# Kernel tuning notes

Hardware: AMD Instinct MI355X
Metric: run time of the kernel (lower is better)

The kernel has to match this reference:

```python
import jax, jax.numpy as jnp
import numpy as np
import math

B, SEQ, H, HKV, D = 2, 2048, 32, 8, 128
BLOCK, LOCAL_BLOCKS, VERT_STRIDE = 64, 16, 8
NB = SEQ // BLOCK


def _build_layout():
    # local + vertical-strided causal block-sparse layout (homo heads),
    # converted from CSR to a padded [NB, max_nnz] column-index table.
    q_idx = np.arange(NB)[:, None]
    k_idx = np.arange(NB)[None, :]
    dense = (k_idx <= q_idx) & ((q_idx - k_idx < LOCAL_BLOCKS) | ((k_idx + 1) % VERT_STRIDE == 0))
    max_nnz = int(dense.sum(1).max())  # == 18 for NB=32, local=16, stride=8
    cols = np.zeros((NB, max_nnz), np.int32)
    valid = np.zeros((NB, max_nnz), np.bool_)
    for i in range(NB):
        c = np.nonzero(dense[i])[0]
        cols[i, :c.size] = c
        valid[i, :c.size] = True
    return jnp.asarray(cols), jnp.asarray(valid)


def setup_inputs() -> dict:
    key = jax.random.key(0)
    kq, kk, kv = jax.random.split(key, 3)
    q = jax.random.normal(kq, (B, SEQ, H, D), jnp.float32)
    k = jax.random.normal(kk, (B, SEQ, HKV, D), jnp.float32)
    v = jax.random.normal(kv, (B, SEQ, HKV, D), jnp.float32)
    layout_cols, layout_mask = _build_layout()
    return {"q": q, "k": k, "v": v, "layout_cols": layout_cols, "layout_mask": layout_mask}


def _attn(q, k, v, layout_cols, layout_mask):
    Bn, S, Hq, Dh = q.shape
    Hkv = k.shape[2]
    g = Hq // Hkv               # GQA group size (q_k_ratio)
    nb, nnz = layout_cols.shape
    blk = S // nb               # block_size
    sm_scale = 1.0 / math.sqrt(Dh)
    # reshape to blocks; keep KV at Hkv heads (no repeat) and group q heads
    qb = q.reshape(Bn, nb, blk, Hkv, g, Dh).transpose(0, 3, 4, 1, 2, 5)  # [B,Hkv,g,nb,blk,D]
    kb = k.reshape(Bn, nb, blk, Hkv, Dh).transpose(0, 3, 1, 2, 4)        # [B,Hkv,nb,blk,D]
    vb = v.reshape(Bn, nb, blk, Hkv, Dh).transpose(0, 3, 1, 2, 4)
    # gather only the attended K/V blocks per query block (honors block sparsity)
    kg = jnp.take(kb, layout_cols, axis=2)  # [B,Hkv,nb,nnz,blk,D]
    vg = jnp.take(vb, layout_cols, axis=2)
    scores = jnp.einsum('bhgqmd,bhqknd->bhgqmkn', qb, kg) * sm_scale  # [B,Hkv,g,nb,blk,nnz,blk]
    # token-level causal mask + padded-column mask (past_len = 0 for prefill)
    q_tok = jnp.arange(nb)[:, None] * blk + jnp.arange(blk)[None, :]            # [nb,blk]
    k_tok = layout_cols[:, :, None] * blk + jnp.arange(blk)[None, None, :]      # [nb,nnz,blk]
    valid = layout_mask[:, None, :, None] & (k_tok[:, None] <= q_tok[:, :, None, None])  # [nb,blk,nnz,blk]
    scores = jnp.where(valid[None, None, None], scores, -jnp.inf)
    p = jax.nn.softmax(scores.reshape(Bn, Hkv, g, nb, blk, nnz * blk), axis=-1).reshape(scores.shape)
    out = jnp.einsum('bhgqmkn,bhqknd->bhgqmd', p, vg)
    return out.transpose(0, 3, 4, 1, 2, 5).reshape(Bn, S, Hq, Dh)


def reference(q, k, v, layout_cols, layout_mask):
    return _attn(q, k, v, layout_cols, layout_mask)
```

## Files before the change

kernel.cpp:

```cpp
#include <hip/hip_runtime.h>

#define B_    2
#define SEQ_  2048
#define H_    32
#define HKV_  8
#define D_    128
#define BLK_  64
#define NB_   32
#define LOCAL_ 16
#define VERT_  8

#define PSTR 72
#define NTASK 512
#define NBLOCK 256

typedef __attribute__((ext_vector_type(8))) short bf16x8;
typedef __attribute__((ext_vector_type(4))) float f32x4;
typedef __attribute__((ext_vector_type(16))) float f32x16;

__device__ __forceinline__ unsigned short f2bf(float f) {
    union { float f; unsigned u; } x; x.f = f;
    unsigned u = x.u;
    return (unsigned short)((u + 0x7FFFu + ((u >> 16) & 1u)) >> 16);
}

__device__ __forceinline__ unsigned pk2(float a, float b) {
#if defined(__has_builtin) && __has_builtin(__builtin_amdgcn_cvt_pk_bf16_f32)
    typedef __attribute__((ext_vector_type(2))) __bf16 bf2;
    bf2 r = __builtin_amdgcn_cvt_pk_bf16_f32(a, b);
    unsigned u; __builtin_memcpy(&u, &r, 4); return u;
#else
    return (unsigned)f2bf(a) | ((unsigned)f2bf(b) << 16);
#endif
}

__device__ __forceinline__ void pswap(unsigned &a, unsigned &b) {
#if defined(__has_builtin) && __has_builtin(__builtin_amdgcn_permlane32_swap)
    auto r = __builtin_amdgcn_permlane32_swap((int)a, (int)b, false, false);
    a = (unsigned)r[0]; b = (unsigned)r[1];
#else
    asm("v_permlane32_swap_b32 %0, %1" : "+v"(a), "+v"(b));
#endif
}

__device__ __forceinline__ f32x16 zero16() {
    f32x16 z;
#pragma unroll
    for (int i = 0; i < 16; ++i) z[i] = 0.f;
    return z;
}

__device__ __forceinline__ int next_valid(int qb, int j) {
    for (++j; j <= qb; ++j)
        if (((qb - j) < LOCAL_) || (((j + 1) & (VERT_ - 1)) == 0)) return j;
    return qb + 1;
}

__device__ __forceinline__ void dma16(const unsigned short* g, unsigned short* l) {
    __builtin_amdgcn_global_load_lds(
        (const __attribute__((address_space(1))) unsigned int*)g,
        (__attribute__((address_space(3))) unsigned int*)l, 16, 0, 0);
}

__global__ __launch_bounds__(256)
void prepass_kernel(const float* __restrict__ kg, const float* __restrict__ vg,
                    unsigned short* __restrict__ Kws, unsigned short* __restrict__ Vws) {
    __shared__ unsigned short Vt[D_ * 72];
    const int bid = blockIdx.x;
    const int b   = bid >> 8;
    const int hkv = (bid >> 5) & 7;
    const int jb  = bid & 31;
    const int tid = threadIdx.x;
    const int rs  = HKV_ * D_;

    const float* kbase = kg + ((size_t)(b * SEQ_ + jb * BLK_) * HKV_ + hkv) * D_;
    const float* vbase = vg + ((size_t)(b * SEQ_ + jb * BLK_) * HKV_ + hkv) * D_;
    unsigned short* Kdst = Kws + ((size_t)(b * 8 + hkv) * SEQ_ + jb * BLK_) * D_;
    unsigned short* Vdst = Vws + ((size_t)(b * 8 + hkv) * NB_ + jb) * (D_ * BLK_);

#pragma unroll
    for (int t = 0; t < 4; ++t) {
        const int q = t * 256 + tid;
        const int row = q >> 4, c = q & 15;
        const float* p = kbase + (size_t)row * rs + c * 8;
        const float4 a = *(const float4*)p;
        const float4 d4 = *(const float4*)(p + 4);
        uint4 u = { pk2(a.x, a.y), pk2(a.z, a.w), pk2(d4.x, d4.y), pk2(d4.z, d4.w) };
        *(uint4*)&Kdst[row * 128 + ((c ^ (row & 15)) << 3)] = u;
    }
#pragma unroll
    for (int t = 0; t < 8; ++t) {
        const int q = t * 256 + tid;
        const int pos = q >> 5, c4 = q & 31;
        const float4 v4 = *(const float4*)(vbase + (size_t)pos * rs + c4 * 4);
        const unsigned u0 = pk2(v4.x, v4.y), u1 = pk2(v4.z, v4.w);
        Vt[(c4 * 4 + 0) * 72 + pos] = (unsigned short)u0;
        Vt[(c4 * 4 + 1) * 72 + pos] = (unsigned short)(u0 >> 16);
        Vt[(c4 * 4 + 2) * 72 + pos] = (unsigned short)u1;
        Vt[(c4 * 4 + 3) * 72 + pos] = (unsigned short)(u1 >> 16);
    }
    __syncthreads();
#pragma unroll
    for (int t = 0; t < 4; ++t) {
        const int q = t * 256 + tid;
        const int d = q >> 3, c = q & 7;
        const uint2 q0 = *(const uint2*)&Vt[d * 72 + c * 8];
        const uint2 q1 = *(const uint2*)&Vt[d * 72 + c * 8 + 4];
        uint4 u = { q0.x, q0.y, q1.x, q1.y };
        *(uint4*)&Vdst[d * 64 + ((c ^ (d & 7)) << 3)] = u;
    }
}

__global__ __launch_bounds__(512, 2)
void sparse_attn_v3(const float* __restrict__ qg, float* __restrict__ outg,
                    const unsigned short* __restrict__ Kws,
                    const unsigned short* __restrict__ Vws,
                    unsigned* __restrict__ ctr) {
    __shared__ __align__(16) unsigned short Kb[2][BLK_ * D_];
    __shared__ __align__(16) unsigned short Vb[2][D_ * BLK_];
    __shared__ unsigned taskLds;

    const int tid  = threadIdx.x;
    const int wave = tid >> 6;
    const int lane = tid & 63;
    const int q5   = lane & 31;
    const int h    = lane >> 5;
    const int hsub = wave >> 1;
    const int rt2  = wave & 1;

    int cskA[8];
#pragma unroll
    for (int dk = 0; dk < 8; ++dk) cskA[dk] = ((((dk * 2) | h) ^ (lane & 15)) << 3);
    int csvB[4];
#pragma unroll
    for (int kc = 0; kc < 4; ++kc) csvB[kc] = ((((kc * 2) | h) ^ (lane & 7)) << 3);

    const float c2 = 0.12751649736230723f;
    const short oneb = (short)0x3F80;
    const bf16x8 ones = {oneb, oneb, oneb, oneb, oneb, oneb, oneb, oneb};

    for (;;) {
        __syncthreads();
        if (tid == 0) taskLds = atomicAdd(ctr, 1u);
        __syncthreads();
        const unsigned t = taskLds;
        if (t >= NTASK) break;

        const int qb  = 31 - (int)(t >> 4);
        const int bh  = (int)(t & 15);
        const int b   = bh >> 3;
        const int hkv = bh & 7;
        const int head = hkv * 4 + hsub;

        const unsigned short* Kbh = Kws + (size_t)(b * 8 + hkv) * SEQ_ * D_;
        const unsigned short* Vbh = Vws + (size_t)(b * 8 + hkv) * NB_ * (D_ * BLK_);

        int j = next_valid(qb, -1);
        {
            const size_t off = (size_t)j * (BLK_ * D_);
#pragma unroll
            for (int i = 0; i < 2; ++i) {
                dma16(Kbh + off + i * 4096 + tid * 8, &Kb[0][i * 4096 + wave * 512]);
                dma16(Vbh + off + i * 4096 + tid * 8, &Vb[0][i * 4096 + wave * 512]);
            }
        }

        bf16x8 qf[8];
        {
            const int row = qb * BLK_ + rt2 * 32 + q5;
            const float* qp = qg + ((size_t)(b * SEQ_ + row) * H_ + head) * D_ + h * 8;
#pragma unroll
            for (int dk = 0; dk < 8; ++dk) {
                const float4 a = *(const float4*)(qp + dk * 16);
                const float4 c = *(const float4*)(qp + dk * 16 + 4);
                uint4 u = { pk2(a.x, a.y), pk2(a.z, a.w), pk2(c.x, c.y), pk2(c.z, c.w) };
                __builtin_memcpy(&qf[dk], &u, 16);
            }
        }

        f32x16 lacc = zero16();
        f32x16 o_acc[4];
#pragma unroll
        for (int dt = 0; dt < 4; ++dt) o_acc[dt] = zero16();

        __syncthreads();
        int it = 0;
        while (j <= qb) {
            const int jn = next_valid(qb, j);
            const int cur = it & 1;
            if (jn <= qb) {
                const size_t off = (size_t)jn * (BLK_ * D_);
#pragma unroll
                for (int i = 0; i < 2; ++i) {
                    dma16(Kbh + off + i * 4096 + tid * 8, &Kb[cur ^ 1][i * 4096 + wave * 512]);
                    dma16(Vbh + off + i * 4096 + tid * 8, &Vb[cur ^ 1][i * 4096 + wave * 512]);
                }
            }

            const bool diag  = (j == qb);
            const bool diagw = diag && (rt2 == 0);

            const unsigned short* kb = Kb[cur];
            f32x16 s0 = zero16(), s1 = zero16();
            {
                const unsigned short* k0r = kb + q5 * 128;
                const unsigned short* k1r = kb + (32 + q5) * 128;
#pragma unroll
                for (int dk = 0; dk < 8; ++dk) {
                    const bf16x8 kf0 = *(const bf16x8*)(k0r + cskA[dk]);
                    s0 = __builtin_amdgcn_mfma_f32_32x32x16_bf16(kf0, qf[dk], s0, 0, 0, 0);
                }
                if (!diagw) {
#pragma unroll
                    for (int dk = 0; dk < 8; ++dk) {
                        const bf16x8 kf1 = *(const bf16x8*)(k1r + cskA[dk]);
                        s1 = __builtin_amdgcn_mfma_f32_32x32x16_bf16(kf1, qf[dk], s1, 0, 0, 0);
                    }
                }
            }

            if (diag) {
                if (rt2 == 0) {
#pragma unroll
                    for (int r = 0; r < 16; ++r) {
                        const int crow = (r & 3) + 8 * (r >> 2) + 4 * h;
                        if (crow > q5) s0[r] = -INFINITY;
                    }
                } else {
#pragma unroll
                    for (int r = 0; r < 16; ++r) {
                        const int crow = (r & 3) + 8 * (r >> 2) + 4 * h;
                        if (crow > q5) s1[r] = -INFINITY;
                    }
                }
            }

#pragma unroll
            for (int r = 0; r < 16; ++r) s0[r] = exp2f(s0[r] * c2);
            if (!diagw) {
#pragma unroll
                for (int r = 0; r < 16; ++r) s1[r] = exp2f(s1[r] * c2);
            }

            bf16x8 pa[4];
#pragma unroll
            for (int kc = 0; kc < 4; ++kc) {
                if (kc >= 2 && diagw) continue;
                const f32x16 &pp = (kc >= 2) ? s1 : s0;
                const int b0 = (kc & 1) * 8;
                unsigned A0 = pk2(pp[b0 + 0], pp[b0 + 1]);
                unsigned B0 = pk2(pp[b0 + 4], pp[b0 + 5]);
                unsigned A1 = pk2(pp[b0 + 2], pp[b0 + 3]);
                unsigned B1 = pk2(pp[b0 + 6], pp[b0 + 7]);
                pswap(A0, B0);
                pswap(A1, B1);
                uint4 u = { A0, A1, B0, B1 };
                __builtin_memcpy(&pa[kc], &u, 16);
                lacc = __builtin_amdgcn_mfma_f32_32x32x16_bf16(pa[kc], ones, lacc, 0, 0, 0);
            }

            const unsigned short* vb = Vb[cur];
#pragma unroll
            for (int dt = 0; dt < 4; ++dt) {
                const unsigned short* vrow = vb + (dt * 32 + q5) * 64;
#pragma unroll
                for (int kc = 0; kc < 4; ++kc) {
                    if (kc >= 2 && diagw) continue;
                    const bf16x8 vf = *(const bf16x8*)(vrow + csvB[kc]);
                    o_acc[dt] = __builtin_amdgcn_mfma_f32_32x32x16_bf16(pa[kc], vf, o_acc[dt], 0, 0, 0);
                }
            }

            __syncthreads();
            j = jn; ++it;
        }

        const int rowbase = qb * BLK_ + rt2 * 32;
#pragma unroll
        for (int r = 0; r < 16; ++r) {
            const int row = rowbase + (r & 3) + 8 * (r >> 2) + 4 * h;
            const float inv = 1.0f / lacc[r];
            float* op = outg + ((size_t)(b * SEQ_ + row) * H_ + head) * D_ + q5;
            op[0]  = o_acc[0][r] * inv;
            op[32] = o_acc[1][r] * inv;
            op[64] = o_acc[2][r] * inv;
            op[96] = o_acc[3][r] * inv;
        }
    }
}

#define KSTR 136
#define VSTR 72
__global__ __launch_bounds__(1024)
void sparse_attn_v1(const float* __restrict__ qg, const float* __restrict__ kg,
                    const float* __restrict__ vg, float* __restrict__ outg,
                    unsigned* __restrict__ ctr) {
    __shared__ __align__(16) unsigned short Klds[BLK_ * KSTR];
    __shared__ __align__(16) unsigned short Vlds[D_ * VSTR];
    __shared__ __align__(16) unsigned short Plds[16 * 16 * PSTR];
    __shared__ unsigned taskLds;

    const int tid  = threadIdx.x;
    const int wave = tid >> 6;
    const int lane = tid & 63;
    const int l15  = lane & 15;
    const int quad = lane >> 4;
    const int hsub = wave >> 2;
    const int rt   = wave & 3;

    const int srow0 = tid >> 5, srow1 = srow0 + 32;
    const int sc4   = tid & 31;
    const int kld0  = srow0 * KSTR + sc4 * 4, kld1 = srow1 * KSTR + sc4 * 4;
    const int vd    = sc4 * 4;
    const int vskew = (sc4 & 7) << 3;
    const int vp0   = (srow0 + vskew) & 63, vp1 = (srow1 + vskew) & 63;
    const size_t stoff0 = (size_t)srow0 * (HKV_ * D_) + sc4 * 4;
    const size_t stoff1 = (size_t)srow1 * (HKV_ * D_) + sc4 * 4;

    const float c2 = 0.12751649736230723f;
    const short oneb = (short)0x3F80;
    const bf16x8 ones = {oneb, oneb, oneb, oneb, oneb, oneb, oneb, oneb};
    unsigned short* pl = &Plds[wave * 16 * PSTR];

    for (;;) {
        __syncthreads();
        if (tid == 0) taskLds = atomicAdd(ctr, 1u);
        __syncthreads();
        const unsigned t = taskLds;
        if (t >= NTASK) break;
        const int qb  = 31 - (int)(t >> 4);
        const int bh  = (int)(t & 15);
        const int b   = bh >> 3;
        const int hkv = bh & 7;
        const int head = hkv * 4 + hsub;
        const float* kbase = kg + ((size_t)(b * SEQ_) * HKV_ + hkv) * D_;
        const float* vbase = vg + ((size_t)(b * SEQ_) * HKV_ + hkv) * D_;
        bf16x8 qf[4];
        {
            const int row = qb * BLK_ + rt * 16 + l15;
            const float* qp = qg + ((size_t)(b * SEQ_ + row) * H_ + head) * D_;
#pragma unroll
            for (int s = 0; s < 4; ++s) {
                const float4 a = *(const float4*)(qp + s * 32 + quad * 8);
                const float4 c = *(const float4*)(qp + s * 32 + quad * 8 + 4);
                uint4 u = { pk2(a.x, a.y), pk2(a.z, a.w), pk2(c.x, c.y), pk2(c.z, c.w) };
                __builtin_memcpy(&qf[s], &u, 16);
            }
        }
        f32x4 lacc = f32x4{0.f, 0.f, 0.f, 0.f};
        f32x4 o_acc[8];
#pragma unroll
        for (int t8 = 0; t8 < 8; ++t8) o_acc[t8] = f32x4{0.f, 0.f, 0.f, 0.f};
        int j = next_valid(qb, -1);
        float4 kpr0, kpr1, vpr0, vpr1;
        {
            const float* kp = kbase + (size_t)j * BLK_ * HKV_ * D_;
            const float* vp = vbase + (size_t)j * BLK_ * HKV_ * D_;
            kpr0 = *(const float4*)(kp + stoff0); kpr1 = *(const float4*)(kp + stoff1);
            vpr0 = *(const float4*)(vp + stoff0); vpr1 = *(const float4*)(vp + stoff1);
        }
        while (j <= qb) {
            const int jn = next_valid(qb, j);
            __syncthreads();
            {
                uint2 u0 = { pk2(kpr0.x, kpr0.y), pk2(kpr0.z, kpr0.w) };
                uint2 u1 = { pk2(kpr1.x, kpr1.y), pk2(kpr1.z, kpr1.w) };
                *(uint2*)&Klds[kld0] = u0;
                *(uint2*)&Klds[kld1] = u1;
                unsigned a0 = pk2(vpr0.x, vpr0.y), a1 = pk2(vpr0.z, vpr0.w);
                Vlds[(vd + 0) * VSTR + vp0] = (unsigned short)a0;
                Vlds[(vd + 1) * VSTR + vp0] = (unsigned short)(a0 >> 16);
                Vlds[(vd + 2) * VSTR + vp0] = (unsigned short)a1;
                Vlds[(vd + 3) * VSTR + vp0] = (unsigned short)(a1 >> 16);
                unsigned b0 = pk2(vpr1.x, vpr1.y), b1 = pk2(vpr1.z, vpr1.w);
                Vlds[(vd + 0) * VSTR + vp1] = (unsigned short)b0;
                Vlds[(vd + 1) * VSTR + vp1] = (unsigned short)(b0 >> 16);
                Vlds[(vd + 2) * VSTR + vp1] = (unsigned short)b1;
                Vlds[(vd + 3) * VSTR + vp1] = (unsigned short)(b1 >> 16);
            }
            __syncthreads();
            if (jn <= qb) {
                const float* kp = kbase + (size_t)jn * BLK_ * HKV_ * D_;
                const float* vp = vbase + (size_t)jn * BLK_ * HKV_ * D_;
                kpr0 = *(const float4*)(kp + stoff0); kpr1 = *(const float4*)(kp + stoff1);
                vpr0 = *(const float4*)(vp + stoff0); vpr1 = *(const float4*)(vp + stoff1);
            }
            f32x4 sacc[4];
#pragma unroll
            for (int t4 = 0; t4 < 4; ++t4) {
                f32x4 acc = f32x4{0.f, 0.f, 0.f, 0.f};
#pragma unroll
                for (int s = 0; s < 4; ++s) {
                    const bf16x8 kf = *(const bf16x8*)&Klds[(t4 * 16 + l15) * KSTR + s * 32 + quad * 8];
                    acc = __builtin_amdgcn_mfma_f32_16x16x32_bf16(qf[s], kf, acc, 0, 0, 0);
                }
                sacc[t4] = acc;
            }
            if (j == qb) {
                const int rowbase = rt * 16 + quad * 4;
#pragma unroll
                for (int t4 = 0; t4 < 4; ++t4) {
                    const int col = t4 * 16 + l15;
#pragma unroll
                    for (int r = 0; r < 4; ++r)
                        if (col > rowbase + r) sacc[t4][r] = -INFINITY;
                }
            }
#pragma unroll
            for (int t4 = 0; t4 < 4; ++t4) {
                const float p0 = exp2f(sacc[t4][0] * c2);
                const float p1 = exp2f(sacc[t4][1] * c2);
                const float p2 = exp2f(sacc[t4][2] * c2);
                const float p3 = exp2f(sacc[t4][3] * c2);
                const unsigned u01 = pk2(p0, p1), u23 = pk2(p2, p3);
                const int cb = t4 * 16 + l15;
                pl[(quad * 4 + 0) * PSTR + cb] = (unsigned short)u01;
                pl[(quad * 4 + 1) * PSTR + cb] = (unsigned short)(u01 >> 16);
                pl[(quad * 4 + 2) * PSTR + cb] = (unsigned short)u23;
                pl[(quad * 4 + 3) * PSTR + cb] = (unsigned short)(u23 >> 16);
            }
#pragma unroll
            for (int s2 = 0; s2 < 2; ++s2) {
                const bf16x8 pf = *(const bf16x8*)&pl[l15 * PSTR + s2 * 32 + quad * 8];
                lacc = __builtin_amdgcn_mfma_f32_16x16x32_bf16(pf, ones, lacc, 0, 0, 0);
                const int k0 = s2 * 32 + quad * 8;
#pragma unroll
                for (int t8 = 0; t8 < 8; ++t8) {
                    const int n  = t8 * 16 + l15;
                    const int p2 = (k0 + (((n >> 2) & 7) << 3)) & 63;
                    const bf16x8 vf = *(const bf16x8*)&Vlds[n * VSTR + p2];
                    o_acc[t8] = __builtin_amdgcn_mfma_f32_16x16x32_bf16(pf, vf, o_acc[t8], 0, 0, 0);
                }
            }
            j = jn;
        }
        const int orow = qb * BLK_ + rt * 16 + quad * 4;
#pragma unroll
        for (int r = 0; r < 4; ++r) {
            const float inv_l = 1.0f / lacc[r];
            float* op = outg + ((size_t)(b * SEQ_ + orow + r) * H_ + head) * D_;
#pragma unroll
            for (int t8 = 0; t8 < 8; ++t8)
                op[t8 * 16 + l15] = o_acc[t8][r] * inv_l;
        }
    }
}

extern "C" void kernel_launch(void* const* d_in, const int* in_sizes, int n_in,
                              void* d_out, int out_size, void* d_ws, size_t ws_size,
                              hipStream_t stream) {
    const float* q = (const float*)d_in[0];
    const float* k = (const float*)d_in[1];
    const float* v = (const float*)d_in[2];
    float* out = (float*)d_out;

    const size_t kws_elems = (size_t)B_ * HKV_ * SEQ_ * D_;
    const size_t need = 256 + 2 * kws_elems * sizeof(unsigned short);
    if (ws_size >= need) {
        unsigned short* Kws = (unsigned short*)((char*)d_ws + 256);
        unsigned short* Vws = Kws + kws_elems;
        hipMemsetAsync(d_ws, 0, 256, stream);
        prepass_kernel<<<dim3(B_ * HKV_ * NB_), dim3(256), 0, stream>>>(k, v, Kws, Vws);
        sparse_attn_v3<<<dim3(NBLOCK), dim3(512), 0, stream>>>(q, out, Kws, Vws, (unsigned*)d_ws);
    } else {
        hipMemsetAsync(d_ws, 0, sizeof(unsigned), stream);
        sparse_attn_v1<<<dim3(NBLOCK), dim3(1024), 0, stream>>>(q, k, v, out, (unsigned*)d_ws);
    }
}
```

Before: 239.8 us.

## Triple-buffer K/V tiles and overlap next QK with current PV

After: 407.7 us. 1.7x slower.

```diff
diff --git a/kernel.cpp b/kernel.cpp
--- a/kernel.cpp
+++ b/kernel.cpp
@@ -112,12 +112,12 @@
 }
 
 __global__ __launch_bounds__(512, 2)
-void sparse_attn_v3(const float* __restrict__ qg, float* __restrict__ outg,
+void sparse_attn_v4(const float* __restrict__ qg, float* __restrict__ outg,
                     const unsigned short* __restrict__ Kws,
                     const unsigned short* __restrict__ Vws,
                     unsigned* __restrict__ ctr) {
-    __shared__ __align__(16) unsigned short Kb[2][BLK_ * D_];
-    __shared__ __align__(16) unsigned short Vb[2][D_ * BLK_];
+    __shared__ __align__(16) unsigned short Kb[3][BLK_ * D_];
+    __shared__ __align__(16) unsigned short Vb[3][D_ * BLK_];
     __shared__ unsigned taskLds;
 
     const int tid  = threadIdx.x;
@@ -155,15 +155,22 @@
         const unsigned short* Kbh = Kws + (size_t)(b * 8 + hkv) * SEQ_ * D_;
         const unsigned short* Vbh = Vws + (size_t)(b * 8 + hkv) * NB_ * (D_ * BLK_);
 
+        auto STAGE = [&](int tile, int buf) {
+            const size_t off = (size_t)tile * (BLK_ * D_);
+#pragma unroll
+            for (int i = 0; i < 2; ++i) {
+                dma16(Kbh + off + i * 4096 + tid * 8, &Kb[buf][i * 4096 + wave * 512]);
+                dma16(Vbh + off + i * 4096 + tid * 8, &Vb[buf][i * 4096 + wave * 512]);
+            }
+        };
+
+        f32x16 lacc = zero16();
+        f32x16 o_acc[4];
+#pragma unroll
+        for (int dt = 0; dt < 4; ++dt) o_acc[dt] = zero16();
+
         int j = next_valid(qb, -1);
-        {
-            const size_t off = (size_t)j * (BLK_ * D_);
-#pragma unroll
-            for (int i = 0; i < 2; ++i) {
-                dma16(Kbh + off + i * 4096 + tid * 8, &Kb[0][i * 4096 + wave * 512]);
-                dma16(Vbh + off + i * 4096 + tid * 8, &Vb[0][i * 4096 + wave * 512]);
-            }
-        }
+        STAGE(j, 0);
 
         bf16x8 qf[8];
         {
@@ -178,47 +185,31 @@
             }
         }
 
-        f32x16 lacc = zero16();
-        f32x16 o_acc[4];
-#pragma unroll
-        for (int dt = 0; dt < 4; ++dt) o_acc[dt] = zero16();
-
-        __syncthreads();
-        int it = 0;
-        while (j <= qb) {
-            const int jn = next_valid(qb, j);
-            const int cur = it & 1;
-            if (jn <= qb) {
-                const size_t off = (size_t)jn * (BLK_ * D_);
-#pragma unroll
-                for (int i = 0; i < 2; ++i) {
-                    dma16(Kbh + off + i * 4096 + tid * 8, &Kb[cur ^ 1][i * 4096 + wave * 512]);
-                    dma16(Vbh + off + i * 4096 + tid * 8, &Vb[cur ^ 1][i * 4096 + wave * 512]);
-                }
-            }
-
-            const bool diag  = (j == qb);
-            const bool diagw = diag && (rt2 == 0);
-
-            const unsigned short* kb = Kb[cur];
-            f32x16 s0 = zero16(), s1 = zero16();
-            {
-                const unsigned short* k0r = kb + q5 * 128;
-                const unsigned short* k1r = kb + (32 + q5) * 128;
+        f32x16 s0, s1;
+        auto QK = [&](int buf, bool skip_hi) {
+            const unsigned short* kb = Kb[buf];
+            const unsigned short* k0r = kb + q5 * 128;
+            const unsigned short* k1r = kb + (32 + q5) * 128;
+            s0 = zero16();
+#pragma unroll
+            for (int dk = 0; dk < 8; ++dk) {
+                const bf16x8 kf0 = *(const bf16x8*)(k0r + cskA[dk]);
+                s0 = __builtin_amdgcn_mfma_f32_32x32x16_bf16(kf0, qf[dk], s0, 0, 0, 0);
+            }
+            if (!skip_hi) {
+                s1 = zero16();
 #pragma unroll
                 for (int dk = 0; dk < 8; ++dk) {
-                    const bf16x8 kf0 = *(const bf16x8*)(k0r + cskA[dk]);
-                    s0 = __builtin_amdgcn_mfma_f32_32x32x16_bf16(kf0, qf[dk], s0, 0, 0, 0);
-                }
-                if (!diagw) {
-#pragma unroll
-                    for (int dk = 0; dk < 8; ++dk) {
-                        const bf16x8 kf1 = *(const bf16x8*)(k1r + cskA[dk]);
-                        s1 = __builtin_amdgcn_mfma_f32_32x32x16_bf16(kf1, qf[dk], s1, 0, 0, 0);
-                    }
-                }
-            }
-
+                    const bf16x8 kf1 = *(const bf16x8*)(k1r + cskA[dk]);
+                    s1 = __builtin_amdgcn_mfma_f32_32x32x16_bf16(kf1, qf[dk], s1, 0, 0, 0);
+                }
+            }
+        };
+
+        bf16x8 pa[4];
+        auto EXPPACK = [&](int jj) {
+            const bool diag = (jj == qb);
+            const bool dw   = diag && (rt2 == 0);
             if (diag) {
                 if (rt2 == 0) {
 #pragma unroll
@@ -234,18 +225,15 @@
                     }
                 }
             }
-
 #pragma unroll
             for (int r = 0; r < 16; ++r) s0[r] = exp2f(s0[r] * c2);
-            if (!diagw) {
+            if (!dw) {
 #pragma unroll
                 for (int r = 0; r < 16; ++r) s1[r] = exp2f(s1[r] * c2);
             }
-
-            bf16x8 pa[4];
 #pragma unroll
             for (int kc = 0; kc < 4; ++kc) {
-                if (kc >= 2 && diagw) continue;
+                if (kc >= 2 && dw) continue;
                 const f32x16 &pp = (kc >= 2) ? s1 : s0;
                 const int b0 = (kc & 1) * 8;
                 unsigned A0 = pk2(pp[b0 + 0], pp[b0 + 1]);
@@ -258,21 +246,37 @@
                 __builtin_memcpy(&pa[kc], &u, 16);
                 lacc = __builtin_amdgcn_mfma_f32_32x32x16_bf16(pa[kc], ones, lacc, 0, 0, 0);
             }
-
-            const unsigned short* vb = Vb[cur];
+        };
+
+        auto PV = [&](int buf, bool dw) {
+            const unsigned short* vb = Vb[buf];
 #pragma unroll
             for (int dt = 0; dt < 4; ++dt) {
                 const unsigned short* vrow = vb + (dt * 32 + q5) * 64;
 #pragma unroll
                 for (int kc = 0; kc < 4; ++kc) {
-                    if (kc >= 2 && diagw) continue;
+                    if (kc >= 2 && dw) continue;
                     const bf16x8 vf = *(const bf16x8*)(vrow + csvB[kc]);
                     o_acc[dt] = __builtin_amdgcn_mfma_f32_32x32x16_bf16(pa[kc], vf, o_acc[dt], 0, 0, 0);
                 }
             }
-
+        };
+
+        int jn = next_valid(qb, j);
+        __syncthreads();
+        if (jn <= qb) STAGE(jn, 1);
+        QK(0, (j == qb) && (rt2 == 0));
+        int it = 0;
+        for (;;) {
+            const bool dw = (j == qb) && (rt2 == 0);
+            EXPPACK(j);
+            if (jn > qb) { PV(it % 3, dw); break; }
             __syncthreads();
-            j = jn; ++it;
+            const int jnn = next_valid(qb, jn);
+            if (jnn <= qb) STAGE(jnn, (it + 2) % 3);
+            QK((it + 1) % 3, (jn == qb) && (rt2 == 0));
+            PV(it % 3, dw);
+            j = jn; jn = jnn; ++it;
         }
 
         const int rowbase = qb * BLK_ + rt2 * 32;
@@ -461,7 +465,7 @@
         unsigned short* Vws = Kws + kws_elems;
         hipMemsetAsync(d_ws, 0, 256, stream);
         prepass_kernel<<<dim3(B_ * HKV_ * NB_), dim3(256), 0, stream>>>(k, v, Kws, Vws);
-        sparse_attn_v3<<<dim3(NBLOCK), dim3(512), 0, stream>>>(q, out, Kws, Vws, (unsigned*)d_ws);
+        sparse_attn_v4<<<dim3(NBLOCK), dim3(512), 0, stream>>>(q, out, Kws, Vws, (unsigned*)d_ws);
     } else {
         hipMemsetAsync(d_ws, 0, sizeof(unsigned), stream);
         sparse_attn_v1<<<dim3(NBLOCK), dim3(1024), 0, stream>>>(q, k, v, out, (unsigned*)d_ws);
```

## Triple-buffer K/V LDS staging with explicit vmcnt waits and single barrier

Applied to the files above, without the earlier changes.

New measurement: 243.5 us. About the same (+1.5%).

```diff
diff --git a/kernel.cpp b/kernel.cpp
--- a/kernel.cpp
+++ b/kernel.cpp
@@ -61,6 +61,9 @@
         (const __attribute__((address_space(1))) unsigned int*)g,
         (__attribute__((address_space(3))) unsigned int*)l, 16, 0, 0);
 }
+
+__device__ __forceinline__ void wait_vm4() { asm volatile("s_waitcnt vmcnt(4)" ::: "memory"); }
+__device__ __forceinline__ void wait_vm0() { asm volatile("s_waitcnt vmcnt(0)" ::: "memory"); }
 
 __global__ __launch_bounds__(256)
 void prepass_kernel(const float* __restrict__ kg, const float* __restrict__ vg,
@@ -112,12 +115,12 @@
 }
 
 __global__ __launch_bounds__(512, 2)
-void sparse_attn_v3(const float* __restrict__ qg, float* __restrict__ outg,
+void sparse_attn_v6(const float* __restrict__ qg, float* __restrict__ outg,
                     const unsigned short* __restrict__ Kws,
                     const unsigned short* __restrict__ Vws,
                     unsigned* __restrict__ ctr) {
-    __shared__ __align__(16) unsigned short Kb[2][BLK_ * D_];
-    __shared__ __align__(16) unsigned short Vb[2][D_ * BLK_];
+    __shared__ __align__(16) unsigned short Kb[3][BLK_ * D_];
+    __shared__ __align__(16) unsigned short Vb[3][D_ * BLK_];
     __shared__ unsigned taskLds;
 
     const int tid  = threadIdx.x;
@@ -155,15 +158,20 @@
         const unsigned short* Kbh = Kws + (size_t)(b * 8 + hkv) * SEQ_ * D_;
         const unsigned short* Vbh = Vws + (size_t)(b * 8 + hkv) * NB_ * (D_ * BLK_);
 
-        int j = next_valid(qb, -1);
-        {
-            const size_t off = (size_t)j * (BLK_ * D_);
+        auto STAGE = [&](int tile, int buf) {
+            const size_t off = (size_t)tile * (BLK_ * D_);
 #pragma unroll
             for (int i = 0; i < 2; ++i) {
-                dma16(Kbh + off + i * 4096 + tid * 8, &Kb[0][i * 4096 + wave * 512]);
-                dma16(Vbh + off + i * 4096 + tid * 8, &Vb[0][i * 4096 + wave * 512]);
-            }
-        }
+                dma16(Kbh + off + i * 4096 + tid * 8, &Kb[buf][i * 4096 + wave * 512]);
+                dma16(Vbh + off + i * 4096 + tid * 8, &Vb[buf][i * 4096 + wave * 512]);
+            }
+        };
+
+        int j  = next_valid(qb, -1);
+        int jn = next_valid(qb, j);
+
+        STAGE(j, 0);
+        __builtin_amdgcn_sched_barrier(0);
 
         bf16x8 qf[8];
         {
@@ -178,29 +186,29 @@
             }
         }
 
+        __builtin_amdgcn_sched_barrier(0);
+        if (jn <= qb) STAGE(jn, 1);
+        __builtin_amdgcn_sched_barrier(0);
+
         f32x16 lacc = zero16();
         f32x16 o_acc[4];
 #pragma unroll
         for (int dt = 0; dt < 4; ++dt) o_acc[dt] = zero16();
 
-        __syncthreads();
         int it = 0;
         while (j <= qb) {
-            const int jn = next_valid(qb, j);
-            const int cur = it & 1;
-            if (jn <= qb) {
-                const size_t off = (size_t)jn * (BLK_ * D_);
-#pragma unroll
-                for (int i = 0; i < 2; ++i) {
-                    dma16(Kbh + off + i * 4096 + tid * 8, &Kb[cur ^ 1][i * 4096 + wave * 512]);
-                    dma16(Vbh + off + i * 4096 + tid * 8, &Vb[cur ^ 1][i * 4096 + wave * 512]);
-                }
-            }
+            const int jnn = next_valid(qb, jn);
+
+            if (jn <= qb) wait_vm4(); else wait_vm0();
+            __builtin_amdgcn_s_barrier();
+            __builtin_amdgcn_sched_barrier(0);
+            if (jnn <= qb) STAGE(jnn, (it + 2) % 3);
+            __builtin_amdgcn_sched_barrier(0);
 
             const bool diag  = (j == qb);
             const bool diagw = diag && (rt2 == 0);
 
-            const unsigned short* kb = Kb[cur];
+            const unsigned short* kb = Kb[it % 3];
             f32x16 s0 = zero16(), s1 = zero16();
             {
                 const unsigned short* k0r = kb + q5 * 128;
@@ -259,7 +267,7 @@
                 lacc = __builtin_amdgcn_mfma_f32_32x32x16_bf16(pa[kc], ones, lacc, 0, 0, 0);
             }
 
-            const unsigned short* vb = Vb[cur];
+            const unsigned short* vb = Vb[it % 3];
 #pragma unroll
             for (int dt = 0; dt < 4; ++dt) {
                 const unsigned short* vrow = vb + (dt * 32 + q5) * 64;
@@ -271,8 +279,7 @@
                 }
             }
 
-            __syncthreads();
-            j = jn; ++it;
+            j = jn; jn = jnn; ++it;
         }
 
         const int rowbase = qb * BLK_ + rt2 * 32;
@@ -461,7 +468,7 @@
         unsigned short* Vws = Kws + kws_elems;
         hipMemsetAsync(d_ws, 0, 256, stream);
         prepass_kernel<<<dim3(B_ * HKV_ * NB_), dim3(256), 0, stream>>>(k, v, Kws, Vws);
-        sparse_attn_v3<<<dim3(NBLOCK), dim3(512), 0, stream>>>(q, out, Kws, Vws, (unsigned*)d_ws);
+        sparse_attn_v6<<<dim3(NBLOCK), dim3(512), 0, stream>>>(q, out, Kws, Vws, (unsigned*)d_ws);
     } else {
         hipMemsetAsync(d_ws, 0, sizeof(unsigned), stream);
         sparse_attn_v1<<<dim3(NBLOCK), dim3(1024), 0, stream>>>(q, k, v, out, (unsigned*)d_ws);
```
